# Performance work log

Measured on AMD Instinct MI355X. Metric: run time of the kernel, lower is better.

Reference implementation:

```python
import jax, jax.numpy as jnp
import numpy as np

N_NODES = 50000
N_EDGES = 800000
IN_CH = 8
CH = 128
EATTR = 6
N_BBOX = 2000
N_CLASSES = 32
N_BLOCKS = 3  # head + 2 residual blocks; n_blocks_out = 3
FUSION = CH * N_BLOCKS  # 384


def _kaiming(key, shape):
    fan_in = shape[0]
    return jax.random.normal(key, shape, dtype=jnp.float32) * np.sqrt(2.0 / fan_in)


def setup_inputs() -> dict:
    key = jax.random.key(0)
    ks = jax.random.split(key, 24)
    x = jax.random.normal(ks[0], (N_NODES, IN_CH), dtype=jnp.float32)
    e_attr = jax.random.normal(ks[1], (N_EDGES, EATTR), dtype=jnp.float32)
    edge = jax.random.randint(ks[2], (2, N_EDGES), 0, N_NODES, dtype=jnp.int32)
    bbox_idx = jnp.sort(jax.random.randint(ks[3], (N_NODES,), 0, N_BBOX, dtype=jnp.int32))
    d_head = 2 * IN_CH + EATTR   # 22
    d_blk = 2 * CH + EATTR       # 262
    inp = {
        "x": x, "e_attr": e_attr,
        "W_h": _kaiming(ks[4], (d_head, CH)), "b_h": jnp.zeros((CH,), jnp.float32),
        "Ws_h": _kaiming(ks[5], (d_head, CH)), "bs_h": jnp.zeros((CH,), jnp.float32),
        "Wb": jnp.stack([_kaiming(ks[6], (d_blk, CH)), _kaiming(ks[7], (d_blk, CH))]),
        "bb": jnp.zeros((2, CH), jnp.float32),
        "Wbs": jnp.stack([_kaiming(ks[8], (d_blk, CH)), _kaiming(ks[9], (d_blk, CH))]),
        "bbs": jnp.zeros((2, CH), jnp.float32),
        "W_f": _kaiming(ks[10], (FUSION, 1024)), "b_f": jnp.zeros((1024,), jnp.float32),
        "W_fs": _kaiming(ks[11], (FUSION, 1024)), "b_fs": jnp.zeros((1024,), jnp.float32),
        "W1": _kaiming(ks[12], ((FUSION + 1024) * 2, 512)), "b1": jnp.zeros((512,), jnp.float32),
        "W2": _kaiming(ks[13], (512, 256)), "b2": jnp.zeros((256,), jnp.float32),
        "W3": _kaiming(ks[14], (256, N_CLASSES)), "b3": jnp.zeros((N_CLASSES,), jnp.float32),
        "edge": edge, "bbox_idx": bbox_idx,
    }
    return inp


def _seg_max0(h, idx, n):
    m = jax.ops.segment_max(h, idx, num_segments=n)
    return jnp.where(jnp.isneginf(m), 0.0, m)  # empty segments -> 0 (torch_scatter semantics)


def _seg_mean(h, idx, n):
    s = jax.ops.segment_sum(h, idx, num_segments=n)
    c = jax.ops.segment_sum(jnp.ones((h.shape[0], 1), h.dtype), idx, num_segments=n)
    return s / jnp.maximum(c, 1.0)


def _graph_conv(x, x_node, src, dst, e_attr, W, b, Ws, bs, n):
    # edge message: MLP(concat(x_i, x_j - x_i, e_attr)); max-scatter for node stream,
    # mean-scatter for super stream (gp2 = two global-pool reductions)
    h = jax.nn.relu(jnp.concatenate([x[src], x[dst] - x[src], e_attr], axis=1) @ W + b)
    f = _seg_max0(h, dst, n)
    hs = jax.nn.relu(jnp.concatenate([x_node[src], x_node[dst] - x_node[src], e_attr], axis=1) @ Ws + bs)
    f_super = _seg_mean(hs, dst, n)
    return f, f_super


def reference(x, e_attr, W_h, b_h, Ws_h, bs_h, Wb, bb, Wbs, bbs,
              W_f, b_f, W_fs, b_fs, W1, b1, W2, b2, W3, b3, edge, bbox_idx):
    src, dst = edge[0], edge[1]
    n = x.shape[0]
    # head conv
    f, fs = _graph_conv(x, x, src, dst, e_attr, W_h, b_h, Ws_h, bs_h, n)
    feats, feats_super = [f], [fs]
    # residual blocks
    for i in range(N_BLOCKS - 1):
        g, gs = _graph_conv(feats[-1], feats_super[-1], src, dst, e_attr,
                            Wb[i], bb[i], Wbs[i], bbs[i], n)
        feats.append(g + feats[-1])
        feats_super.append(gs + feats_super[-1])
    feats = jnp.concatenate(feats, axis=1)              # [N, 384]
    fusion = jax.nn.relu(feats @ W_f + b_f)             # [N, 1024]
    out_feat = jnp.concatenate([fusion, feats], axis=1) # [N, 1408]
    feats_super = jnp.concatenate(feats_super, axis=1)  # [N, 384]
    feats_super = _seg_mean(feats_super, bbox_idx, N_BBOX)            # [B, 384]
    fusion_super = jax.nn.relu(feats_super @ W_fs + b_fs)             # [B, 1024]
    out_super = jnp.concatenate([fusion_super, feats_super], axis=1)  # [B, 1408]
    pooled = _seg_max0(out_feat, bbox_idx, N_BBOX)                    # [B, 1408]
    h = jnp.concatenate([pooled, out_super], axis=1)                  # [B, 2816]
    h = jax.nn.relu(h @ W1 + b1)
    h = jax.nn.relu(h @ W2 + b2)  # dropout=0 / eval mode
    logits = h @ W3 + b3          # classifier == 'softmax': raw logits returned
    return logits
```

## Files before the change

### kernel.cpp

```cpp
#include <hip/hip_runtime.h>

#define NN      50000
#define NE      800000
#define INCH    8
#define CH      128
#define EA      6
#define NB      2000
#define NB_PAD  2048
#define NCLS    32
#define FUS     384
#define K1      2816
#define SCAN_NBLK 49

typedef _Float16 half8 __attribute__((ext_vector_type(8)));
typedef _Float16 h2 __attribute__((ext_vector_type(2)));
typedef float f32x4 __attribute__((ext_vector_type(4)));

__global__ __launch_bounds__(256) void k_deg(const int* __restrict__ edge,
                                             int* __restrict__ deg) {
  int e = blockIdx.x * 256 + threadIdx.x;
  if (e < NE) atomicAdd(&deg[edge[NE + e]], 1);
}

__global__ __launch_bounds__(1024) void k_scan1(const int* __restrict__ deg,
                                                int* __restrict__ row_ptr,
                                                int* __restrict__ bsum) {
  __shared__ int wsum[16];
  const int t = threadIdx.x, lane = t & 63, w = t >> 6;
  const int i = blockIdx.x * 1024 + t;
  int x = (i < NN) ? deg[i] : 0;
#pragma unroll
  for (int off = 1; off < 64; off <<= 1) {
    int y = __shfl_up(x, off, 64);
    if (lane >= off) x += y;
  }
  if (lane == 63) wsum[w] = x;
  __syncthreads();
  if (w == 0 && lane < 16) {
    int s = wsum[lane];
#pragma unroll
    for (int off = 1; off < 16; off <<= 1) {
      int y = __shfl_up(s, off, 64);
      if (lane >= off) s += y;
    }
    wsum[lane] = s;
  }
  __syncthreads();
  int incl = x + ((w == 0) ? 0 : wsum[w - 1]);
  if (i < NN) row_ptr[i + 1] = incl;
  if (t == 1023) bsum[blockIdx.x] = incl;
}

__global__ __launch_bounds__(64) void k_scan2(int* __restrict__ bsum) {
  const int t = threadIdx.x;
  int x = (t < SCAN_NBLK) ? bsum[t] : 0;
#pragma unroll
  for (int off = 1; off < 64; off <<= 1) {
    int y = __shfl_up(x, off, 64);
    if (t >= off) x += y;
  }
  int ex = __shfl_up(x, 1, 64);
  if (t == 0) ex = 0;
  if (t < SCAN_NBLK) bsum[t] = ex;
}

__global__ __launch_bounds__(256) void k_scan3(const int* __restrict__ bsum,
                                               int* __restrict__ row_ptr) {
  const int i = blockIdx.x * 256 + threadIdx.x;
  if (i == 0) row_ptr[0] = 0;
  if (i < NN) row_ptr[i + 1] += bsum[i >> 10];
}

__global__ __launch_bounds__(256) void k_fill(
    const int* __restrict__ edge, const float* __restrict__ eattr,
    const int* __restrict__ row_ptr, int* __restrict__ cursor,
    int* __restrict__ ssrc, _Float16* __restrict__ sea8) {
  int e = blockIdx.x * 256 + threadIdx.x;
  if (e >= NE) return;
  int s = edge[e], d = edge[NE + e];
  int idx = row_ptr[d] + atomicAdd(&cursor[d], 1);
  ssrc[idx] = s;
  half8 v;
#pragma unroll
  for (int j = 0; j < EA; ++j) v[j] = (_Float16)eattr[(size_t)e * EA + j];
  v[6] = (_Float16)0.f; v[7] = (_Float16)0.f;
  *(half8*)(sea8 + (size_t)idx * 8) = v;
}

__global__ __launch_bounds__(256) void k_segstart(const int* __restrict__ bbox,
                                                  int* __restrict__ seg) {
  int i = blockIdx.x * 256 + threadIdx.x;
  if (i >= NN) return;
  int bc = bbox[i];
  int bp = (i == 0) ? -1 : bbox[i - 1];
  for (int j = bp + 1; j <= bc; ++j) seg[j] = i;
  if (i == NN - 1)
    for (int j = bc + 1; j <= NB; ++j) seg[j] = NN;
}

__global__ __launch_bounds__(256) void k_node_pq(
    const float* __restrict__ X, int ldx, int K,
    const float* __restrict__ W, const float* __restrict__ bias,
    _Float16* __restrict__ PQi, _Float16* __restrict__ Qi, int sel) {
  const int t = threadIdx.x, lane = t & 63, wv = t >> 6;
  const int nbase = blockIdx.x * 32 + wv * 8;
  const int c = lane * 2;
  const float2 bv = *(const float2*)(bias + c);
  float2 pacc[8], qacc[8];
#pragma unroll
  for (int u = 0; u < 8; ++u) { pacc[u] = bv; qacc[u] = make_float2(0.f, 0.f); }
  const int xrow = min(nbase + (lane >> 3), NN - 1);
  const int xk = lane & 7;
  for (int k0 = 0; k0 < K; k0 += 8) {
    const float xv = X[(size_t)xrow * ldx + k0 + xk];
#pragma unroll
    for (int j = 0; j < 8; ++j) {
      const float2 w1 = *(const float2*)(W + (size_t)(k0 + j) * CH + c);
      const float2 w2 = *(const float2*)(W + (size_t)(K + k0 + j) * CH + c);
      const float2 wd = {w1.x - w2.x, w1.y - w2.y};
#pragma unroll
      for (int u = 0; u < 8; ++u) {
        const float xs = __shfl(xv, u * 8 + j, 64);
        pacc[u].x += xs * wd.x; pacc[u].y += xs * wd.y;
        qacc[u].x += xs * w2.x; qacc[u].y += xs * w2.y;
      }
    }
  }
#pragma unroll
  for (int u = 0; u < 8; ++u) {
    const int node = nbase + u;
    if (node < NN) {
      const size_t o = ((size_t)node * 64 + lane) * 4 + sel * 2;
      *(h2*)(PQi + o) = (h2){(_Float16)pacc[u].x, (_Float16)pacc[u].y};
      *(h2*)(Qi + o)  = (h2){(_Float16)qacc[u].x, (_Float16)qacc[u].y};
    }
  }
}

__global__ __launch_bounds__(64) void k_cvtWnpq(
    const float* __restrict__ WN, const float* __restrict__ WS,
    _Float16* __restrict__ whN, _Float16* __restrict__ whS) {
  const float* W = blockIdx.y ? WS : WN;
  _Float16* wh   = blockIdx.y ? whS : whN;
  const int c = blockIdx.x >> 4, tile = blockIdx.x & 15;
  const int L = threadIdx.x;
  const int n = tile * 16 + (L & 15);
  const int k0 = c * 32 + (L >> 4) * 8;
  half8 v;
#pragma unroll
  for (int j = 0; j < 8; ++j) {
    const int k = k0 + j;
    float val;
    if (n < CH) val = W[(size_t)k * CH + n] - W[(size_t)(CH + k) * CH + n];
    else        val = W[(size_t)(CH + k) * CH + (n - CH)];
    v[j] = (_Float16)val;
  }
  *(half8*)(wh + (((size_t)(c * 16 + tile)) * 64 + L) * 8) = v;
}

__global__ __launch_bounds__(256) void k_npq_mfma(
    const float* __restrict__ Xn, const float* __restrict__ Xs, int ldx,
    const _Float16* __restrict__ whN, const _Float16* __restrict__ whS,
    const float* __restrict__ biasN, const float* __restrict__ biasS,
    _Float16* __restrict__ PQi, _Float16* __restrict__ Qi) {
  const int sel = blockIdx.y;
  const float* X = sel ? Xs : Xn;
  const _Float16* wh = sel ? whS : whN;
  const float* bias = sel ? biasS : biasN;
  const int t = threadIdx.x, lane = t & 63, wv = t >> 6;
  const int nbase = blockIdx.x * 64;
  const int m = lane & 15, quad = lane >> 4;
  f32x4 acc[4][4];
#pragma unroll
  for (int i = 0; i < 4; ++i)
#pragma unroll
    for (int nt = 0; nt < 4; ++nt) acc[i][nt] = (f32x4){0.f, 0.f, 0.f, 0.f};
#pragma unroll
  for (int ks = 0; ks < 4; ++ks) {
    half8 b[4];
#pragma unroll
    for (int nt = 0; nt < 4; ++nt)
      b[nt] = *(const half8*)(wh + (((size_t)(ks * 16 + wv * 4 + nt)) * 64 + lane) * 8);
#pragma unroll
    for (int i = 0; i < 4; ++i) {
      const int row = min(nbase + i * 16 + m, NN - 1);
      const float* src = X + (size_t)row * ldx + ks * 32 + quad * 8;
      const float4 f0 = *(const float4*)src;
      const float4 f1 = *(const float4*)(src + 4);
      half8 a;
      a[0] = (_Float16)f0.x; a[1] = (_Float16)f0.y;
      a[2] = (_Float16)f0.z; a[3] = (_Float16)f0.w;
      a[4] = (_Float16)f1.x; a[5] = (_Float16)f1.y;
      a[6] = (_Float16)f1.z; a[7] = (_Float16)f1.w;
#pragma unroll
      for (int nt = 0; nt < 4; ++nt)
        acc[i][nt] = __builtin_amdgcn_mfma_f32_16x16x32_f16(a, b[nt], acc[i][nt],
                                                            0, 0, 0);
    }
  }
#pragma unroll
  for (int i = 0; i < 4; ++i)
#pragma unroll
    for (int nt = 0; nt < 4; ++nt) {
      const int col = wv * 64 + nt * 16 + m;
      const float bv = (col < CH) ? bias[col] : 0.f;
#pragma unroll
      for (int r = 0; r < 4; ++r) {
        const int row = nbase + i * 16 + quad * 4 + r;
        if (row < NN) {
          const float v = acc[i][nt][r] + bv;
          if (col < CH)
            PQi[((size_t)row * 64 + (col >> 1)) * 4 + sel * 2 + (col & 1)] =
                (_Float16)v;
          else {
            const int qc = col - CH;
            Qi[((size_t)row * 64 + (qc >> 1)) * 4 + sel * 2 + (qc & 1)] =
                (_Float16)v;
          }
        }
      }
    }
}

__global__ __launch_bounds__(256) void k_conv2(
    const int* __restrict__ row_ptr, const int* __restrict__ ssrc,
    const _Float16* __restrict__ sea8,
    const _Float16* __restrict__ PQi, const _Float16* __restrict__ Qi,
    const float* __restrict__ Cn, const float* __restrict__ Cs,
    float* __restrict__ feats, float* __restrict__ sfeats,
    int cur, int prev) {
  const int t = threadIdx.x;
  const int lane = t & 63;
  const int node = blockIdx.x * 4 + (t >> 6);
  const int c = lane * 2;
  h2 cwnh[EA], cwsh[EA];
#pragma unroll
  for (int j = 0; j < EA; ++j) {
    const float2 a = *(const float2*)(Cn + j * CH + c);
    const float2 b = *(const float2*)(Cs + j * CH + c);
    cwnh[j] = (h2){(_Float16)a.x, (_Float16)a.y};
    cwsh[j] = (h2){(_Float16)b.x, (_Float16)b.y};
  }
  int i0 = __builtin_amdgcn_readfirstlane(row_ptr[node]);
  int i1 = __builtin_amdgcn_readfirstlane(row_ptr[node + 1]);
  const uint2 qv = *(const uint2*)(Qi + ((size_t)node * 64 + lane) * 4);
  const h2 qnh = *(const h2*)&qv.x;
  const h2 qsh = *(const h2*)&qv.y;
  const _Float16* pqL = PQi + (size_t)lane * 4;
  h2 anh = (h2){(_Float16)0.f, (_Float16)0.f};
  float as0 = 0.f, as1 = 0.f;
  const h2 zero = (h2){(_Float16)0.f, (_Float16)0.f};
#define COMP(PV, J)                                                        \
  {                                                                        \
    unsigned w0 = __shfl((int)ea_l.x, (J), 64);                            \
    unsigned w1 = __shfl((int)ea_l.y, (J), 64);                            \
    unsigned w2 = __shfl((int)ea_l.z, (J), 64);                            \
    const h2 ea01 = *(const h2*)&w0;                                       \
    const h2 ea23 = *(const h2*)&w1;                                       \
    const h2 ea45 = *(const h2*)&w2;                                       \
    h2 vn = *(const h2*)&PV.x + qnh;                                       \
    h2 vs = *(const h2*)&PV.y + qsh;                                       \
    h2 b;                                                                  \
    b = (h2){ea01[0], ea01[0]}; vn += b * cwnh[0]; vs += b * cwsh[0];      \
    b = (h2){ea01[1], ea01[1]}; vn += b * cwnh[1]; vs += b * cwsh[1];      \
    b = (h2){ea23[0], ea23[0]}; vn += b * cwnh[2]; vs += b * cwsh[2];      \
    b = (h2){ea23[1], ea23[1]}; vn += b * cwnh[3]; vs += b * cwsh[3];      \
    b = (h2){ea45[0], ea45[0]}; vn += b * cwnh[4]; vs += b * cwsh[4];      \
    b = (h2){ea45[1], ea45[1]}; vn += b * cwnh[5]; vs += b * cwsh[5];      \
    anh = __builtin_elementwise_max(anh, vn);                              \
    const h2 vsr = __builtin_elementwise_max(vs, zero);                    \
    as0 += (float)vsr[0]; as1 += (float)vsr[1];                            \
  }
  for (int base = i0; base < i1; base += 64) {
    const int cnt = min(64, i1 - base);
    int s_l = 0;
    uint4 ea_l = {0u, 0u, 0u, 0u};
    if (lane < cnt) {
      s_l = ssrc[base + lane];
      ea_l = *(const uint4*)(sea8 + (size_t)(base + lane) * 8);
    }
    int j = 0;
    for (; j + 4 <= cnt; j += 4) {
      const int sa = __shfl(s_l, j, 64);
      const int sb = __shfl(s_l, j + 1, 64);
      const int sc = __shfl(s_l, j + 2, 64);
      const int sd = __shfl(s_l, j + 3, 64);
      const uint2 pva = *(const uint2*)(pqL + (size_t)sa * 256);
      const uint2 pvb = *(const uint2*)(pqL + (size_t)sb * 256);
      const uint2 pvc = *(const uint2*)(pqL + (size_t)sc * 256);
      const uint2 pvd = *(const uint2*)(pqL + (size_t)sd * 256);
      COMP(pva, j) COMP(pvb, j + 1) COMP(pvc, j + 2) COMP(pvd, j + 3)
    }
    for (; j < cnt; ++j) {
      const int sa = __shfl(s_l, j, 64);
      const uint2 pva = *(const uint2*)(pqL + (size_t)sa * 256);
      COMP(pva, j)
    }
  }
#undef COMP
  float an0 = (float)anh[0], an1 = (float)anh[1];
  const float inv = 1.f / fmaxf((float)(i1 - i0), 1.f);
  as0 *= inv; as1 *= inv;
  const size_t o = (size_t)node * FUS + (size_t)cur * CH + c;
  if (prev >= 0) {
    const size_t op = (size_t)node * FUS + (size_t)prev * CH + c;
    const float2 prn = *(const float2*)(feats + op);
    const float2 prs = *(const float2*)(sfeats + op);
    an0 += prn.x; an1 += prn.y;
    as0 += prs.x; as1 += prs.y;
  }
  float2 on = {an0, an1}, os = {as0, as1};
  *(float2*)(feats + o) = on;
  *(float2*)(sfeats + o) = os;
}

__global__ __launch_bounds__(64) void k_cvtApack(const float* __restrict__ feats,
                                                 _Float16* __restrict__ ap) {
  const int rb = blockIdx.x / 12, ks = blockIdx.x % 12;
  const int L = threadIdx.x, m = L & 15, quad = L >> 4;
#pragma unroll
  for (int i = 0; i < 4; ++i) {
    const int row = rb * 64 + i * 16 + m;
    const int rowc = min(row, NN - 1);
    const float* src = feats + (size_t)rowc * FUS + ks * 32 + quad * 8;
    half8 v;
    if (row < NN) {
      const float4 f0 = *(const float4*)src;
      const float4 f1 = *(const float4*)(src + 4);
      v[0] = (_Float16)f0.x; v[1] = (_Float16)f0.y;
      v[2] = (_Float16)f0.z; v[3] = (_Float16)f0.w;
      v[4] = (_Float16)f1.x; v[5] = (_Float16)f1.y;
      v[6] = (_Float16)f1.z; v[7] = (_Float16)f1.w;
    } else {
#pragma unroll
      for (int j = 0; j < 8; ++j) v[j] = (_Float16)0.f;
    }
    *(half8*)(ap + (((size_t)(rb * 12 + ks) * 4 + i) * 64 + L) * 8) = v;
  }
}

template <int N, int NT>
__global__ __launch_bounds__(64) void k_cvtB(const float* __restrict__ W,
                                             _Float16* __restrict__ wh) {
  const int c = blockIdx.x / NT;
  const int tile = blockIdx.x % NT;
  const int L = threadIdx.x;
  const int n = tile * 16 + (L & 15);
  const int k0 = c * 32 + (L >> 4) * 8;
  half8 v;
#pragma unroll
  for (int j = 0; j < 8; ++j) v[j] = (_Float16)W[(size_t)(k0 + j) * N + n];
  *(half8*)(wh + (((size_t)(c * NT + tile)) * 64 + L) * 8) = v;
}

__global__ __launch_bounds__(256, 8) void k_pool_mfma(
    const _Float16* __restrict__ aP, const _Float16* __restrict__ wh,
    const int* __restrict__ bbox, const float* __restrict__ bf,
    float* __restrict__ pooled) {
  __shared__ float cl[32 * 132];
  __shared__ int s_bb[64];
  const int t = threadIdx.x, lane = t & 63, wv = t >> 6;
  const int fid = blockIdx.x;
  const int xcd = fid & 7, slot = fid >> 3;
  const int cg = slot & 7;
  const int rb = xcd * 98 + (slot >> 3);
  const int nbase = rb * 64;
  const int m = lane & 15, quad = lane >> 4;
  if (t < 64) s_bb[t] = bbox[min(nbase + t, NN - 1)];
  f32x4 acc[4][2];
#pragma unroll
  for (int i = 0; i < 4; ++i)
#pragma unroll
    for (int nt = 0; nt < 2; ++nt) acc[i][nt] = (f32x4){0.f, 0.f, 0.f, 0.f};
  const _Float16* apb = aP + (size_t)rb * 12 * 2048 + (size_t)lane * 8;
  const _Float16* bp = wh + ((size_t)(cg * 8 + wv * 2) * 64 + lane) * 8;
#pragma unroll
  for (int ks = 0; ks < 12; ++ks) {
    const half8 b0 = *(const half8*)(bp + (size_t)ks * 32768);
    const half8 b1 = *(const half8*)(bp + (size_t)ks * 32768 + 512);
#pragma unroll
    for (int i = 0; i < 4; ++i) {
      const half8 a = *(const half8*)(apb + ((size_t)ks * 4 + i) * 512);
      acc[i][0] = __builtin_amdgcn_mfma_f32_16x16x32_f16(a, b0, acc[i][0], 0, 0, 0);
      acc[i][1] = __builtin_amdgcn_mfma_f32_16x16x32_f16(a, b1, acc[i][1], 0, 0, 0);
    }
  }
  const int col = t & 127, rh = t >> 7;
  const int gcol = cg * 128 + col;
  const float bias = bf[gcol];
#pragma unroll
  for (int p = 0; p < 2; ++p) {
    __syncthreads();
#pragma unroll
    for (int ii = 0; ii < 2; ++ii)
#pragma unroll
      for (int nt = 0; nt < 2; ++nt) {
        const int scol = wv * 32 + nt * 16 + m;
#pragma unroll
        for (int r = 0; r < 4; ++r)
          cl[(ii * 16 + quad * 4 + r) * 132 + scol] = acc[p * 2 + ii][nt][r];
      }
    __syncthreads();
    int curb = -1;
    float mx = 0.f;
    for (int rr = 0; rr < 16; ++rr) {
      const int rl = rh * 16 + rr;
      const int node = nbase + p * 32 + rl;
      if (node >= NN) break;
      const int bid = s_bb[p * 32 + rl];
      const float v = fmaxf(cl[rl * 132 + col] + bias, 0.f);
      if (bid != curb) {
        if (curb >= 0)
          atomicMax((unsigned*)(pooled + (size_t)curb * 1408 + gcol),
                    __float_as_uint(mx));
        curb = bid;
        mx = v;
      } else {
        mx = fmaxf(mx, v);
      }
    }
    if (curb >= 0)
      atomicMax((unsigned*)(pooled + (size_t)curb * 1408 + gcol),
                __float_as_uint(mx));
  }
}

__global__ __launch_bounds__(256) void k_poolraw(
    const float* __restrict__ feats, const float* __restrict__ sfeats,
    const int* __restrict__ seg, float* __restrict__ pooled,
    float* __restrict__ sb) {
  const int b = blockIdx.x, t = threadIdx.x;
  if (t >= 192) return;
  const int c2 = t * 2;
  const int n0 = __builtin_amdgcn_readfirstlane(seg[b]);
  const int n1 = __builtin_amdgcn_readfirstlane(seg[b + 1]);
  float2 fmx = {0.f, 0.f}, ss = {0.f, 0.f};
  for (int n = n0; n < n1; ++n) {
    const float2 f2 = *(const float2*)(feats + (size_t)n * FUS + c2);
    fmx.x = fmaxf(fmx.x, f2.x); fmx.y = fmaxf(fmx.y, f2.y);
    const float2 s2 = *(const float2*)(sfeats + (size_t)n * FUS + c2);
    ss.x += s2.x; ss.y += s2.y;
  }
  *(float2*)(pooled + (size_t)b * 1408 + 1024 + c2) = fmx;
  const float inv = 1.f / fmaxf((float)(n1 - n0), 1.f);
  float2 o = {ss.x * inv, ss.y * inv};
  *(float2*)(sb + (size_t)b * FUS + c2) = o;
}

__global__ __launch_bounds__(256) void k_fusion_super(
    const float* __restrict__ sb, const float* __restrict__ Wfs,
    const float* __restrict__ bfs, float* __restrict__ fs) {
  const int t = threadIdx.x, lane = t & 63, wv = t >> 6;
  const int r0 = blockIdx.x * 4;
  const int c = (blockIdx.y * 4 + wv) * 128 + lane * 2;
  float2 acc[4];
#pragma unroll
  for (int u = 0; u < 4; ++u) acc[u] = make_float2(0.f, 0.f);
  const int xr = r0 + (lane >> 4), xk = lane & 15;
  for (int k0 = 0; k0 < FUS; k0 += 16) {
    const float xv = sb[(size_t)xr * FUS + k0 + xk];
#pragma unroll
    for (int j = 0; j < 16; ++j) {
      const float2 w = *(const float2*)(Wfs + (size_t)(k0 + j) * 1024 + c);
#pragma unroll
      for (int u = 0; u < 4; ++u) {
        const float xs = __shfl(xv, u * 16 + j, 64);
        acc[u].x += xs * w.x; acc[u].y += xs * w.y;
      }
    }
  }
  const float2 b = *(const float2*)(bfs + c);
#pragma unroll
  for (int u = 0; u < 4; ++u) {
    float2 o = {fmaxf(acc[u].x + b.x, 0.f), fmaxf(acc[u].y + b.y, 0.f)};
    *(float2*)(fs + (size_t)(r0 + u) * 1024 + c) = o;
  }
}

__global__ __launch_bounds__(256) void k_cvt_cat(
    const float* __restrict__ pooled, const float* __restrict__ fsup,
    const float* __restrict__ sb, _Float16* __restrict__ bbH) {
  const size_t off = ((size_t)blockIdx.x * 256 + threadIdx.x) * 8;
  const int row = (int)(off / K1);
  const int col = (int)(off - (size_t)row * K1);
  half8 v;
  if (row < NB) {
    const float* src;
    if (col < 1408)      src = pooled + (size_t)row * 1408 + col;
    else if (col < 2432) src = fsup + (size_t)row * 1024 + (col - 1408);
    else                 src = sb + (size_t)row * FUS + (col - 2432);
    const float4 f0 = *(const float4*)src;
    const float4 f1 = *(const float4*)(src + 4);
    v[0] = (_Float16)f0.x; v[1] = (_Float16)f0.y;
    v[2] = (_Float16)f0.z; v[3] = (_Float16)f0.w;
    v[4] = (_Float16)f1.x; v[5] = (_Float16)f1.y;
    v[6] = (_Float16)f1.z; v[7] = (_Float16)f1.w;
  } else {
#pragma unroll
    for (int j = 0; j < 8; ++j) v[j] = (_Float16)0.f;
  }
  *(half8*)(bbH + off) = v;
}

__global__ __launch_bounds__(256) void k_mlp1_mfma(
    const _Float16* __restrict__ bbH, const _Float16* __restrict__ wh,
    const float* __restrict__ b1, float* __restrict__ h1) {
  const int t = threadIdx.x, lane = t & 63, wv = t >> 6;
  const int nbase = blockIdx.x * 64;
  const int cg = blockIdx.y;
  const int m = lane & 15, quad = lane >> 4;
  f32x4 acc[4][2];
#pragma unroll
  for (int i = 0; i < 4; ++i)
#pragma unroll
    for (int nt = 0; nt < 2; ++nt) acc[i][nt] = (f32x4){0.f, 0.f, 0.f, 0.f};
  const _Float16* ap = bbH + (size_t)(nbase + m) * K1 + quad * 8;
  const _Float16* bp = wh + ((size_t)(cg * 8 + wv * 2) * 64 + lane) * 8;
#pragma unroll 4
  for (int ks = 0; ks < 88; ++ks) {
    const half8 b0 = *(const half8*)(bp + (size_t)ks * 16384);
    const half8 b1v = *(const half8*)(bp + (size_t)ks * 16384 + 512);
#pragma unroll
    for (int i = 0; i < 4; ++i) {
      const half8 a = *(const half8*)(ap + (size_t)(i * 16) * K1 + ks * 32);
      acc[i][0] = __builtin_amdgcn_mfma_f32_16x16x32_f16(a, b0, acc[i][0], 0, 0, 0);
      acc[i][1] = __builtin_amdgcn_mfma_f32_16x16x32_f16(a, b1v, acc[i][1], 0, 0, 0);
    }
  }
#pragma unroll
  for (int i = 0; i < 4; ++i)
#pragma unroll
    for (int nt = 0; nt < 2; ++nt) {
      const int gcol = cg * 128 + wv * 32 + nt * 16 + m;
      const float bias = b1[gcol];
#pragma unroll
      for (int r = 0; r < 4; ++r) {
        const int row = nbase + i * 16 + quad * 4 + r;
        if (row < NB)
          h1[(size_t)row * 512 + gcol] = fmaxf(acc[i][nt][r] + bias, 0.f);
      }
    }
}

__global__ __launch_bounds__(256) void k_mlp2(
    const float* __restrict__ h1, const float* __restrict__ W2,
    const float* __restrict__ b2, float* __restrict__ h2o) {
  const int r0 = blockIdx.x * 8, t = threadIdx.x;
  float acc[8];
#pragma unroll
  for (int u = 0; u < 8; ++u) acc[u] = 0.f;
  for (int k = 0; k < 512; ++k) {
    float w = W2[(size_t)k * 256 + t];
#pragma unroll
    for (int u = 0; u < 8; ++u) acc[u] += h1[(size_t)(r0 + u) * 512 + k] * w;
  }
  float bv = b2[t];
#pragma unroll
  for (int u = 0; u < 8; ++u)
    h2o[(size_t)(r0 + u) * 256 + t] = fmaxf(acc[u] + bv, 0.f);
}

__global__ __launch_bounds__(256) void k_mlp3(
    const float* __restrict__ h2i, const float* __restrict__ W3,
    const float* __restrict__ b3, float* __restrict__ out) {
  const int r0 = blockIdx.x * 8, t = threadIdx.x;
  const int u = t >> 5, oc = t & 31;
  const float* x = h2i + (size_t)(r0 + u) * 256;
  float acc = 0.f;
  for (int k = 0; k < 256; ++k) acc += x[k] * W3[(size_t)k * 32 + oc];
  out[(size_t)(r0 + u) * 32 + oc] = acc + b3[oc];
}

extern "C" void kernel_launch(void* const* d_in, const int* in_sizes, int n_in,
                              void* d_out, int out_size, void* d_ws, size_t ws_size,
                              hipStream_t stream) {
  const float* x     = (const float*)d_in[0];
  const float* eattr = (const float*)d_in[1];
  const float* W_h   = (const float*)d_in[2];
  const float* b_h   = (const float*)d_in[3];
  const float* Ws_h  = (const float*)d_in[4];
  const float* bs_h  = (const float*)d_in[5];
  const float* Wb    = (const float*)d_in[6];
  const float* bb    = (const float*)d_in[7];
  const float* Wbs   = (const float*)d_in[8];
  const float* bbs   = (const float*)d_in[9];
  const float* W_f   = (const float*)d_in[10];
  const float* b_f   = (const float*)d_in[11];
  const float* W_fs  = (const float*)d_in[12];
  const float* b_fs  = (const float*)d_in[13];
  const float* W1    = (const float*)d_in[14];
  const float* b1    = (const float*)d_in[15];
  const float* W2    = (const float*)d_in[16];
  const float* b2    = (const float*)d_in[17];
  const float* W3    = (const float*)d_in[18];
  const float* b3    = (const float*)d_in[19];
  const int*   edge  = (const int*)d_in[20];
  const int*   bbox  = (const int*)d_in[21];
  float* out = (float*)d_out;

  float* p = (float*)d_ws;
  float* feats  = p; p += (size_t)NN * FUS;
  float* sfeats = p; p += (size_t)NN * FUS;
  float* PQ     = p; p += (size_t)2 * NN * CH;
  _Float16* PQi = (_Float16*)PQ;
  _Float16* Qi  = PQi + (size_t)NN * 256;
  _Float16* aPack = (_Float16*)PQ;
  _Float16* WfH   = aPack + (size_t)784 * 12 * 2048;
  float* pooled   = (float*)(WfH + (size_t)FUS * 1024);
  float* sb   = PQ;
  float* fsup = sb + (size_t)NB * FUS;
  float* h1   = fsup + (size_t)NB * 1024;
  float* h2b  = h1 + (size_t)NB * 512;
  _Float16* bbH = (_Float16*)(h2b + (size_t)NB * 256);
  _Float16* W1H = bbH + (size_t)NB_PAD * K1;
  _Float16* sea8 = (_Float16*)p;
  int* ssrc    = (int*)(sea8 + (size_t)NE * 8);
  int* row_ptr = ssrc + NE;
  int* deg     = row_ptr + NN + 1;
  int* cursor  = deg + NN;
  int* seg     = cursor + NN;
  _Float16* WcatN = (_Float16*)(seg + NB + 1);
  _Float16* WcatS = WcatN + (size_t)128 * 256;
  int* bsum = (int*)(WcatS + (size_t)128 * 256);

  hipMemsetAsync(deg, 0, 2 * NN * sizeof(int), stream);

  k_deg<<<(NE + 255) / 256, 256, 0, stream>>>(edge, deg);
  k_scan1<<<SCAN_NBLK, 1024, 0, stream>>>(deg, row_ptr, bsum);
  k_scan2<<<1, 64, 0, stream>>>(bsum);
  k_scan3<<<(NN + 255) / 256, 256, 0, stream>>>(bsum, row_ptr);
  k_fill<<<(NE + 255) / 256, 256, 0, stream>>>(edge, eattr, row_ptr, cursor,
                                               ssrc, sea8);
  k_segstart<<<(NN + 255) / 256, 256, 0, stream>>>(bbox, seg);

  const int npq_grid = (NN + 31) / 32;

  k_node_pq<<<npq_grid, 256, 0, stream>>>(x, INCH, INCH, W_h, b_h, PQi, Qi, 0);
  k_node_pq<<<npq_grid, 256, 0, stream>>>(x, INCH, INCH, Ws_h, bs_h, PQi, Qi, 1);
  k_conv2<<<NN / 4, 256, 0, stream>>>(row_ptr, ssrc, sea8, PQi, Qi,
                                      W_h + 2 * INCH * CH, Ws_h + 2 * INCH * CH,
                                      feats, sfeats, 0, -1);

  for (int i = 0; i < 2; ++i) {
    const float* Wi  = Wb  + (size_t)i * 262 * CH;
    const float* bi  = bb  + (size_t)i * CH;
    const float* Wsi = Wbs + (size_t)i * 262 * CH;
    const float* bsi = bbs + (size_t)i * CH;
    k_cvtWnpq<<<dim3(64, 2), 64, 0, stream>>>(Wi, Wsi, WcatN, WcatS);
    k_npq_mfma<<<dim3((NN + 63) / 64, 2), 256, 0, stream>>>(
        feats + i * CH, sfeats + i * CH, FUS, WcatN, WcatS, bi, bsi, PQi, Qi);
    k_conv2<<<NN / 4, 256, 0, stream>>>(row_ptr, ssrc, sea8, PQi, Qi,
                                        Wi + 2 * CH * CH, Wsi + 2 * CH * CH,
                                        feats, sfeats, i + 1, i);
  }

  k_cvtApack<<<784 * 12, 64, 0, stream>>>(feats, aPack);
  k_cvtB<1024, 64><<<12 * 64, 64, 0, stream>>>(W_f, WfH);
  hipMemsetAsync(pooled, 0, (size_t)NB * 1408 * sizeof(float), stream);
  k_pool_mfma<<<784 * 8, 256, 0, stream>>>(aPack, WfH, bbox, b_f, pooled);
  k_poolraw<<<NB, 256, 0, stream>>>(feats, sfeats, seg, pooled, sb);
  k_fusion_super<<<dim3(NB / 4, 2), 256, 0, stream>>>(sb, W_fs, b_fs, fsup);

  k_cvt_cat<<<(int)(((size_t)NB_PAD * K1 / 8) / 256), 256, 0, stream>>>(
      pooled, fsup, sb, bbH);
  k_cvtB<512, 32><<<88 * 32, 64, 0, stream>>>(W1, W1H);
  k_mlp1_mfma<<<dim3(NB_PAD / 64, 4), 256, 0, stream>>>(bbH, W1H, b1, h1);
  k_mlp2<<<NB / 8, 256, 0, stream>>>(h1, W2, b2, h2b);
  k_mlp3<<<NB / 8, 256, 0, stream>>>(h2b, W3, b3, out);
}
```

Measured before the change: 939.1 us.

## Stage pool GEMM A tiles through LDS with double buffering; merge small launches

The pooled fusion GEMM now loads each A k-slice cooperatively into a double-buffered LDS region and prefetches the next B fragments and A slice while MFMAs run on the current one. Previously each wave read every A fragment from global memory on its own. The change also merges the two node_pq launches into one 2D grid and hoists the weight conversion for both residual blocks into a single launch. The costs are a barrier per k-step and a lower occupancy hint on the pool kernel.

Measured after the change: 901.6 us. -4.0%, faster.

```diff
diff --git a/kernel.cpp b/kernel.cpp
--- a/kernel.cpp
+++ b/kernel.cpp
@@ -100,8 +100,12 @@
 
 __global__ __launch_bounds__(256) void k_node_pq(
     const float* __restrict__ X, int ldx, int K,
-    const float* __restrict__ W, const float* __restrict__ bias,
-    _Float16* __restrict__ PQi, _Float16* __restrict__ Qi, int sel) {
+    const float* __restrict__ WN, const float* __restrict__ bN,
+    const float* __restrict__ WS, const float* __restrict__ bS,
+    _Float16* __restrict__ PQi, _Float16* __restrict__ Qi) {
+  const int sel = blockIdx.y;
+  const float* W = sel ? WS : WN;
+  const float* bias = sel ? bS : bN;
   const int t = threadIdx.x, lane = t & 63, wv = t >> 6;
   const int nbase = blockIdx.x * 32 + wv * 8;
   const int c = lane * 2;
@@ -138,10 +142,11 @@
 }
 
 __global__ __launch_bounds__(64) void k_cvtWnpq(
-    const float* __restrict__ WN, const float* __restrict__ WS,
+    const float* __restrict__ WbAll, const float* __restrict__ WbsAll,
     _Float16* __restrict__ whN, _Float16* __restrict__ whS) {
-  const float* W = blockIdx.y ? WS : WN;
-  _Float16* wh   = blockIdx.y ? whS : whN;
+  const int blk = blockIdx.z;
+  const float* W = (blockIdx.y ? WbsAll : WbAll) + (size_t)blk * 262 * CH;
+  _Float16* wh   = (blockIdx.y ? whS : whN) + (size_t)blk * 32768;
   const int c = blockIdx.x >> 4, tile = blockIdx.x & 15;
   const int L = threadIdx.x;
   const int n = tile * 16 + (L & 15);
@@ -353,12 +358,13 @@
   *(half8*)(wh + (((size_t)(c * NT + tile)) * 64 + L) * 8) = v;
 }
 
-__global__ __launch_bounds__(256, 8) void k_pool_mfma(
+__global__ __launch_bounds__(256, 6) void k_pool_mfma(
     const _Float16* __restrict__ aP, const _Float16* __restrict__ wh,
     const int* __restrict__ bbox, const float* __restrict__ bf,
     float* __restrict__ pooled) {
   __shared__ float cl[32 * 132];
   __shared__ int s_bb[64];
+  _Float16* abuf = (_Float16*)cl;
   const int t = threadIdx.x, lane = t & 63, wv = t >> 6;
   const int fid = blockIdx.x;
   const int xcd = fid & 7, slot = fid >> 3;
@@ -372,18 +378,37 @@
   for (int i = 0; i < 4; ++i)
 #pragma unroll
     for (int nt = 0; nt < 2; ++nt) acc[i][nt] = (f32x4){0.f, 0.f, 0.f, 0.f};
-  const _Float16* apb = aP + (size_t)rb * 12 * 2048 + (size_t)lane * 8;
+  const _Float16* apc = aP + (size_t)rb * 12 * 2048 + (size_t)wv * 512 +
+                        (size_t)lane * 8;
   const _Float16* bp = wh + ((size_t)(cg * 8 + wv * 2) * 64 + lane) * 8;
+  _Float16* wslot = abuf + wv * 512 + lane * 8;
+  const _Float16* rbase = abuf + lane * 8;
+  half8 b0 = *(const half8*)(bp);
+  half8 b1 = *(const half8*)(bp + 512);
+  half8 rA = *(const half8*)(apc);
+  *(half8*)(wslot) = rA;
+  half8 rN = *(const half8*)(apc + 2048);
+  __syncthreads();
 #pragma unroll
   for (int ks = 0; ks < 12; ++ks) {
-    const half8 b0 = *(const half8*)(bp + (size_t)ks * 32768);
-    const half8 b1 = *(const half8*)(bp + (size_t)ks * 32768 + 512);
+    const int cur = ks & 1;
+    half8 nb0, nb1;
+    if (ks < 11) {
+      nb0 = *(const half8*)(bp + (size_t)(ks + 1) * 32768);
+      nb1 = *(const half8*)(bp + (size_t)(ks + 1) * 32768 + 512);
+    }
 #pragma unroll
     for (int i = 0; i < 4; ++i) {
-      const half8 a = *(const half8*)(apb + ((size_t)ks * 4 + i) * 512);
+      const half8 a = *(const half8*)(rbase + cur * 2048 + i * 512);
       acc[i][0] = __builtin_amdgcn_mfma_f32_16x16x32_f16(a, b0, acc[i][0], 0, 0, 0);
       acc[i][1] = __builtin_amdgcn_mfma_f32_16x16x32_f16(a, b1, acc[i][1], 0, 0, 0);
     }
+    if (ks < 11) {
+      *(half8*)(wslot + (cur ^ 1) * 2048) = rN;
+      b0 = nb0; b1 = nb1;
+    }
+    if (ks < 10) rN = *(const half8*)(apc + (size_t)(ks + 2) * 2048);
+    __syncthreads();
   }
   const int col = t & 127, rh = t >> 7;
   const int gcol = cg * 128 + col;
@@ -620,8 +645,8 @@
   int* cursor  = deg + NN;
   int* seg     = cursor + NN;
   _Float16* WcatN = (_Float16*)(seg + NB + 1);
-  _Float16* WcatS = WcatN + (size_t)128 * 256;
-  int* bsum = (int*)(WcatS + (size_t)128 * 256);
+  _Float16* WcatS = WcatN + (size_t)2 * 128 * 256;
+  int* bsum = (int*)(WcatS + (size_t)2 * 128 * 256);
 
   hipMemsetAsync(deg, 0, 2 * NN * sizeof(int), stream);
 
@@ -635,20 +660,21 @@
 
   const int npq_grid = (NN + 31) / 32;
 
-  k_node_pq<<<npq_grid, 256, 0, stream>>>(x, INCH, INCH, W_h, b_h, PQi, Qi, 0);
-  k_node_pq<<<npq_grid, 256, 0, stream>>>(x, INCH, INCH, Ws_h, bs_h, PQi, Qi, 1);
+  k_node_pq<<<dim3(npq_grid, 2), 256, 0, stream>>>(x, INCH, INCH, W_h, b_h,
+                                                   Ws_h, bs_h, PQi, Qi);
   k_conv2<<<NN / 4, 256, 0, stream>>>(row_ptr, ssrc, sea8, PQi, Qi,
                                       W_h + 2 * INCH * CH, Ws_h + 2 * INCH * CH,
                                       feats, sfeats, 0, -1);
 
+  k_cvtWnpq<<<dim3(64, 2, 2), 64, 0, stream>>>(Wb, Wbs, WcatN, WcatS);
   for (int i = 0; i < 2; ++i) {
     const float* Wi  = Wb  + (size_t)i * 262 * CH;
     const float* bi  = bb  + (size_t)i * CH;
     const float* Wsi = Wbs + (size_t)i * 262 * CH;
     const float* bsi = bbs + (size_t)i * CH;
-    k_cvtWnpq<<<dim3(64, 2), 64, 0, stream>>>(Wi, Wsi, WcatN, WcatS);
     k_npq_mfma<<<dim3((NN + 63) / 64, 2), 256, 0, stream>>>(
-        feats + i * CH, sfeats + i * CH, FUS, WcatN, WcatS, bi, bsi, PQi, Qi);
+        feats + i * CH, sfeats + i * CH, FUS, WcatN + (size_t)i * 32768,
+        WcatS + (size_t)i * 32768, bi, bsi, PQi, Qi);
     k_conv2<<<NN / 4, 256, 0, stream>>>(row_ptr, ssrc, sea8, PQi, Qi,
                                         Wi + 2 * CH * CH, Wsi + 2 * CH * CH,
                                         feats, sfeats, i + 1, i);
```
